# Optimization experiments

Hardware: AMD Instinct MI355X
Metric: run time of the kernel (lower is better)

Reference implementation:

```python
import jax, jax.numpy as jnp
import numpy as np

B, S, D, H = 2, 2048, 2048, 16
DH = D // H  # 128
EPS = 1e-6


def _rms_norm(x, w):
    # RMSNorm over last dim with learnable scale
    var = jnp.mean(jnp.square(x), axis=-1, keepdims=True)
    return x * jax.lax.rsqrt(var + EPS) * w


def _apply_rope(x, angles):
    # x: [B, S, H, DH]; angles: [S, DH//2]; interleaved pair rotation
    xs = x.reshape(*x.shape[:-1], DH // 2, 2)
    x0, x1 = xs[..., 0], xs[..., 1]
    cos = jnp.cos(angles)[None, :, None, :]  # [1,S,1,DH/2]
    sin = jnp.sin(angles)[None, :, None, :]
    r0 = x0 * cos - x1 * sin
    r1 = x0 * sin + x1 * cos
    return jnp.stack([r0, r1], axis=-1).reshape(x.shape)


def setup_inputs() -> dict:
    key = jax.random.key(0)
    ks = jax.random.split(key, 4)
    x = jax.random.normal(ks[0], (B, S, D), dtype=jnp.float32)
    # standard RoPE angle table: pos * inv_freq
    inv_freq = 1.0 / (10000.0 ** (jnp.arange(0, DH, 2, dtype=jnp.float32) / DH))
    pos = jnp.arange(S, dtype=jnp.float32)
    rp_freqs = pos[:, None] * inv_freq[None, :]  # [S, DH/2]
    Win = jax.random.normal(ks[1], (3 * D, D), dtype=jnp.float32) * (D ** -0.5)
    b_in = jnp.zeros((3 * D,), dtype=jnp.float32)
    Wout = jax.random.normal(ks[2], (D, D), dtype=jnp.float32) * (D ** -0.5)
    b_out = jnp.zeros((D,), dtype=jnp.float32)
    qk_w = jnp.ones((DH,), dtype=jnp.float32)
    out_w = jnp.ones((D,), dtype=jnp.float32)
    return {"x": x, "rp_freqs": rp_freqs, "Win": Win, "b_in": b_in,
            "Wout": Wout, "b_out": b_out, "qk_w": qk_w, "out_w": out_w}


def reference(x, rp_freqs, Win, b_in, Wout, b_out, qk_w, out_w):
    b, s, d = x.shape
    qkv = jnp.einsum('bsd,ed->bse', x, Win) + b_in  # [B,S,3D]
    qkv = qkv.reshape(b, s, 3, H, DH)
    q, k, v = qkv[:, :, 0], qkv[:, :, 1], qkv[:, :, 2]  # each [B,S,H,DH]
    q = _apply_rope(q, rp_freqs)
    k = _apply_rope(k, rp_freqs)
    q = _rms_norm(q, qk_w)
    k = _rms_norm(k, qk_w)
    # causal SDPA, scale = 1/sqrt(DH) (default)
    a = jax.nn.dot_product_attention(q, k, v, is_causal=True)  # [B,S,H,DH]
    a = a.reshape(b, s, d)
    a = _rms_norm(a, out_w)
    return jnp.einsum('bsd,ed->bse', a, Wout) + b_out
```

## Files before the change

kernel.cpp:

```cpp
#include <hip/hip_runtime.h>
#include <cstdint>
#include <cstddef>

#define Bq  2
#define Sq  2048
#define Dq  2048
#define Hq  16
#define DHq 128
#define E3q 6144

typedef __attribute__((ext_vector_type(8))) short s16x8;
typedef __attribute__((ext_vector_type(4))) float f32x4;

__device__ __forceinline__ unsigned short f2bf(float f){
  union { float f; unsigned u; } v; v.f = f;
  unsigned r = v.u + 0x7FFFu + ((v.u >> 16) & 1u);
  return (unsigned short)(r >> 16);
}
__device__ __forceinline__ float bf2f(unsigned short b){
  union { unsigned u; float f; } v; v.u = ((unsigned)b) << 16;
  return v.f;
}
__device__ __forceinline__ unsigned cvtpk_bf16(float lo, float hi){
  unsigned r;
  asm("v_cvt_pk_bf16_f32 %0, %1, %2" : "=v"(r) : "v"(lo), "v"(hi));
  return r;
}

__device__ __forceinline__ void gload_lds16(const void* g, void* l){
  __builtin_amdgcn_global_load_lds(
      (const __attribute__((address_space(1))) void*)g,
      (__attribute__((address_space(3))) void*)l, 16, 0, 0);
}

__global__ __launch_bounds__(256) void k_convert(const float* __restrict__ in,
                                                 unsigned short* __restrict__ out, int n4){
  int stride = gridDim.x * blockDim.x;
  for (int i = blockIdx.x*blockDim.x + threadIdx.x; i < n4; i += stride){
    float4 v = reinterpret_cast<const float4*>(in)[i];
    ushort4 o;
    o.x = f2bf(v.x); o.y = f2bf(v.y); o.z = f2bf(v.z); o.w = f2bf(v.w);
    reinterpret_cast<ushort4*>(out)[i] = o;
  }
}

__global__ __launch_bounds__(512, 1) void k_gemm1_8ph(const unsigned short* __restrict__ A,
                                                      const unsigned short* __restrict__ Bt,
                                                      const float* __restrict__ bias,
                                                      unsigned short* __restrict__ C){
  const int K = 2048, N = 6144;
  const int bid = blockIdx.x;
  const int xcd = bid & 7, u = bid >> 3;
  const int m0 = (xcd*4 + (u & 3)) * 128;
  const int n0 = (u >> 2) * 384;

  const int tid = threadIdx.x;
  const int lane = tid & 63, w = tid >> 6, g = lane >> 4, c = lane & 15;
  const int wm = w >> 2, wn = w & 3;

  __shared__ __align__(16) unsigned short L[65536];

  const int srow = tid >> 2, spc = tid & 3;
  const int ssw = (spc ^ ((srow >> 1) & 3)) << 3;
  const unsigned short* aSrc  = A  + (size_t)(m0 + srow      )*K + ssw;
  const unsigned short* bSrc0 = Bt + (size_t)(n0 + srow      )*K + ssw;
  const unsigned short* bSrc1 = Bt + (size_t)(n0 + srow + 128)*K + ssw;
  const unsigned short* bSrc2 = Bt + (size_t)(n0 + srow + 256)*K + ssw;

  auto stA = [&](int t, int h){
    gload_lds16(aSrc + t*64 + h*32, &L[((t&1)*2 + h)*4096 + tid*8]);
  };
  auto stB = [&](int t, int h, int uu){
    const unsigned short* s = (uu==0) ? bSrc0 : (uu==1) ? bSrc1 : bSrc2;
    gload_lds16(s + t*64 + h*32, &L[16384 + ((t&1)*2 + h)*12288 + uu*4096 + tid*8]);
  };

  int aoff[4], boff[6];
#pragma unroll
  for (int mf=0; mf<4; ++mf){
    int row = wm*64 + mf*16 + c;
    aoff[mf] = row*32 + ((g ^ ((row>>1)&3)) << 3);
  }
#pragma unroll
  for (int nf=0; nf<6; ++nf){
    int row = wn*96 + nf*16 + c;
    boff[nf] = row*32 + ((g ^ ((row>>1)&3)) << 3);
  }

  f32x4 acc[4][6];
#pragma unroll
  for (int i=0;i<4;i++)
#pragma unroll
    for (int j=0;j<6;j++)
#pragma unroll
      for (int r=0;r<4;r++) acc[i][j][r] = 0.f;

  auto RDA = [&](int b, int h, s16x8* af){
    const int ab = (b*2 + h)*4096;
#pragma unroll
    for (int mf=0; mf<4; ++mf) af[mf] = *(const s16x8*)&L[ab + aoff[mf]];
  };
  auto RDB = [&](int b, int h, int nh, s16x8* bf){
    const int bb = 16384 + (b*2 + h)*12288;
#pragma unroll
    for (int j=0; j<3; ++j) bf[j] = *(const s16x8*)&L[bb + boff[nh*3 + j]];
  };
  auto MM = [&](s16x8* af, s16x8* bf, int nh){
    __builtin_amdgcn_s_setprio(1);
#pragma unroll
    for (int mf=0; mf<4; ++mf)
#pragma unroll
      for (int j=0; j<3; ++j)
        acc[mf][nh*3+j] = __builtin_amdgcn_mfma_f32_16x16x32_bf16(af[mf], bf[j], acc[mf][nh*3+j], 0,0,0);
    __builtin_amdgcn_s_setprio(0);
  };
  auto BAR = [&](){
    __builtin_amdgcn_sched_barrier(0);
    __builtin_amdgcn_s_barrier();
    __builtin_amdgcn_sched_barrier(0);
  };

  stA(0,0); stB(0,0,0); stB(0,0,1); stB(0,0,2);
  stA(0,1); stB(0,1,0); stB(0,1,1); stB(0,1,2);
  stA(1,0); stB(1,0,0); stB(1,0,1); stB(1,0,2);
  asm volatile("s_waitcnt vmcnt(4)" ::: "memory");
  __builtin_amdgcn_s_barrier();

  for (int i=0; i<16; ++i){
    const int T0 = 2*i, T1 = 2*i + 1;
    const bool st = (i < 15);
    s16x8 af[4], bf[3];
    RDA(0,0,af); RDB(0,0,0,bf);
    stA(T1,1); stB(T1,1,0);
    BAR(); MM(af,bf,0); BAR();
    RDB(0,0,1,bf);
    stB(T1,1,1); stB(T1,1,2);
    BAR(); MM(af,bf,1); BAR();
    RDA(0,1,af); RDB(0,1,0,bf);
    if (st){ stA(T0+2,0); stB(T0+2,0,0); }
    BAR(); MM(af,bf,0); BAR();
    RDB(0,1,1,bf);
    if (st){ stB(T0+2,0,1); stB(T0+2,0,2); }
    __builtin_amdgcn_sched_barrier(0);
    if (st) asm volatile("s_waitcnt vmcnt(4)" ::: "memory");
    else    asm volatile("s_waitcnt vmcnt(0)" ::: "memory");
    BAR(); MM(af,bf,1); BAR();
    RDA(1,0,af); RDB(1,0,0,bf);
    if (st){ stA(T0+2,1); stB(T0+2,1,0); }
    BAR(); MM(af,bf,0); BAR();
    RDB(1,0,1,bf);
    if (st){ stB(T0+2,1,1); stB(T0+2,1,2); }
    BAR(); MM(af,bf,1); BAR();
    RDA(1,1,af); RDB(1,1,0,bf);
    if (st){ stA(T1+2,0); stB(T1+2,0,0); }
    BAR(); MM(af,bf,0); BAR();
    RDB(1,1,1,bf);
    if (st){ stB(T1+2,0,1); stB(T1+2,0,2); }
    __builtin_amdgcn_sched_barrier(0);
    if (st) asm volatile("s_waitcnt vmcnt(4)" ::: "memory");
    else    asm volatile("s_waitcnt vmcnt(0)" ::: "memory");
    BAR(); MM(af,bf,1); BAR();
  }

#pragma unroll
  for (int nf=0; nf<6; ++nf){
    const int col = n0 + wn*96 + nf*16 + c;
    const float bv = bias[col];
#pragma unroll
    for (int mf=0; mf<4; ++mf){
      const int row = m0 + wm*64 + mf*16 + g*4;
#pragma unroll
      for (int r=0; r<4; ++r)
        C[(size_t)(row+r)*N + col] = f2bf(acc[mf][nf][r] + bv);
    }
  }
}

template<int F32OUT>
__global__ __launch_bounds__(256, 2) void k_gemm_bt(const unsigned short* __restrict__ A,
                                                    const unsigned short* __restrict__ Bt,
                                                    const float* __restrict__ bias,
                                                    void* __restrict__ C,
                                                    int M, int N, int K){
  const int bid = blockIdx.x;
  const int xcd = bid & 7, u = bid >> 3;
  const int by = xcd*4 + (u & 3);
  const int bx = u >> 2;
  const int m0 = by * 128, n0 = bx * 256;

  const int tid = threadIdx.x;
  const int w = tid >> 6, lane = tid & 63, g = lane >> 4, c = lane & 15;

  __shared__ __align__(16) unsigned short L[3 * 12288];

  const int NT = K >> 5;

  const int r0 = tid >> 2, pc = tid & 3;
  const unsigned short* Ab0 = &A [(size_t)(m0 + r0      )*K + (size_t)((pc ^ (((r0      )>>1)&3))*8)];
  const unsigned short* Ab1 = &A [(size_t)(m0 + r0 +  64)*K + (size_t)((pc ^ (((r0 + 64)>>1)&3))*8)];
  const unsigned short* Bb0 = &Bt[(size_t)(n0 + r0      )*K + (size_t)((pc ^ (((r0      )>>1)&3))*8)];
  const unsigned short* Bb1 = &Bt[(size_t)(n0 + r0 +  64)*K + (size_t)((pc ^ (((r0 + 64)>>1)&3))*8)];
  const unsigned short* Bb2 = &Bt[(size_t)(n0 + r0 + 128)*K + (size_t)((pc ^ (((r0 +128)>>1)&3))*8)];
  const unsigned short* Bb3 = &Bt[(size_t)(n0 + r0 + 192)*K + (size_t)((pc ^ (((r0 +192)>>1)&3))*8)];

  auto stage = [&](int tile, int slot){
    const int kt = tile << 5;
    unsigned short* Ls = &L[slot * 12288];
    gload_lds16(Ab0 + kt, &Ls[tid*8]);
    gload_lds16(Ab1 + kt, &Ls[(tid+256)*8]);
    gload_lds16(Bb0 + kt, &Ls[4096 + tid*8]);
    gload_lds16(Bb1 + kt, &Ls[4096 + (tid+256)*8]);
    gload_lds16(Bb2 + kt, &Ls[4096 + (tid+512)*8]);
    gload_lds16(Bb3 + kt, &Ls[4096 + (tid+768)*8]);
  };

  f32x4 acc[8][4];
#pragma unroll
  for (int i=0;i<8;i++)
#pragma unroll
    for (int j=0;j<4;j++)
#pragma unroll
      for (int r=0;r<4;r++) acc[i][j][r] = 0.f;

  int aoff[8], boff[4];
#pragma unroll
  for (int mi=0;mi<8;mi++){
    int row = mi*16 + c;
    aoff[mi] = row*32 + ((g ^ ((row>>1)&3)) << 3);
  }
#pragma unroll
  for (int ni=0;ni<4;ni++){
    int row = w*64 + ni*16 + c;
    boff[ni] = 4096 + row*32 + ((g ^ ((row>>1)&3)) << 3);
  }

  stage(0,0); stage(1,1);

  int slot = 0;
  for (int t = 0; t < NT; ++t){
    if (t < NT-1) asm volatile("s_waitcnt vmcnt(6)" ::: "memory");
    else          asm volatile("s_waitcnt vmcnt(0)" ::: "memory");
    __builtin_amdgcn_s_barrier();
    __builtin_amdgcn_sched_barrier(0);
    if (t+2 < NT) stage(t+2, slot == 0 ? 2 : slot-1);

    const unsigned short* Ls = &L[slot * 12288];
    s16x8 bfr[4];
#pragma unroll
    for (int ni=0;ni<4;ni++) bfr[ni] = *(const s16x8*)&Ls[boff[ni]];
    __builtin_amdgcn_s_setprio(1);
#pragma unroll
    for (int mi=0;mi<8;mi++){
      s16x8 af = *(const s16x8*)&Ls[aoff[mi]];
#pragma unroll
      for (int ni=0;ni<4;ni++)
        acc[mi][ni] = __builtin_amdgcn_mfma_f32_16x16x32_bf16(af, bfr[ni], acc[mi][ni], 0,0,0);
    }
    __builtin_amdgcn_s_setprio(0);
    slot = (slot == 2) ? 0 : slot+1;
  }

#pragma unroll
  for (int ni=0;ni<4;ni++){
    const int col = n0 + w*64 + ni*16 + c;
    const float bv = bias[col];
#pragma unroll
    for (int mi=0;mi<8;mi++){
      const int row = m0 + mi*16 + g*4;
#pragma unroll
      for (int r=0;r<4;r++){
        float v = acc[mi][ni][r] + bv;
        if (F32OUT) ((float*)C)[(size_t)(row+r)*N + col] = v;
        else ((unsigned short*)C)[(size_t)(row+r)*N + col] = f2bf(v);
      }
    }
  }
}

__global__ __launch_bounds__(256) void k_rope_qk(const unsigned short* __restrict__ QKV,
                                                 const float* __restrict__ rp,
                                                 const float* __restrict__ qk_w,
                                                 unsigned short* __restrict__ Qp,
                                                 unsigned short* __restrict__ Kp){
  const int p = threadIdx.x;
  const int s = blockIdx.x*4 + threadIdx.y;
  const int h = blockIdx.y;
  const int b = blockIdx.z;
  const size_t n = (size_t)b*Sq + s;
  const int bh = b*Hq + h;

  float ang = rp[s*64 + p];
  float sn, cs; sincosf(ang, &sn, &cs);
  float w0 = qk_w[2*p], w1 = qk_w[2*p+1];
  const float QSCALE = 0.08838834764831845f * 1.4426950408889634f;

  {
    unsigned q01 = *(const unsigned*)&QKV[n*E3q + h*DHq + 2*p];
    float x0 = bf2f((unsigned short)(q01 & 0xFFFFu));
    float x1 = bf2f((unsigned short)(q01 >> 16));
    float r0 = x0*cs - x1*sn, r1 = x0*sn + x1*cs;
    float ss = r0*r0 + r1*r1;
#pragma unroll
    for (int m=1;m<64;m<<=1) ss += __shfl_xor(ss, m);
    float sc = rsqrtf(ss/128.f + 1e-6f) * QSCALE;
    unsigned short o0 = f2bf(r0*sc*w0), o1 = f2bf(r1*sc*w1);
    *(unsigned*)&Qp[((size_t)bh*Sq + s)*DHq + 2*p] = (unsigned)o0 | ((unsigned)o1<<16);
  }
  {
    unsigned k01 = *(const unsigned*)&QKV[n*E3q + Dq + h*DHq + 2*p];
    float x0 = bf2f((unsigned short)(k01 & 0xFFFFu));
    float x1 = bf2f((unsigned short)(k01 >> 16));
    float r0 = x0*cs - x1*sn, r1 = x0*sn + x1*cs;
    float ss = r0*r0 + r1*r1;
#pragma unroll
    for (int m=1;m<64;m<<=1) ss += __shfl_xor(ss, m);
    float sc = rsqrtf(ss/128.f + 1e-6f);
    unsigned short o0 = f2bf(r0*sc*w0), o1 = f2bf(r1*sc*w1);
    *(unsigned*)&Kp[((size_t)bh*Sq + s)*DHq + 2*p] = (unsigned)o0 | ((unsigned)o1<<16);
  }
}

__global__ __launch_bounds__(256) void k_transpose_v(const unsigned short* __restrict__ QKV,
                                                     unsigned short* __restrict__ Vt){
  const int sblk = blockIdx.x;
  const int bh = blockIdx.y;
  const int b = bh >> 4, h = bh & 15;
  const int tid = threadIdx.x;
  __shared__ unsigned short T[128][136];

  const size_t base = ((size_t)(b*Sq) + sblk*128) * E3q + 2*(size_t)Dq + h*DHq;
#pragma unroll
  for (int i=0;i<8;i++){
    int pk = tid + i*256;
    int row = pk >> 4, cc = (pk & 15) * 8;
    s16x8 v = *(const s16x8*)&QKV[base + (size_t)row*E3q + cc];
    *(s16x8*)&T[row][cc] = v;
  }
  __syncthreads();
  const int dh = tid >> 1, sh = (tid & 1) * 64;
  unsigned short buf[64];
#pragma unroll
  for (int s=0;s<64;s++) buf[s] = T[sh + s][dh];
  size_t obase = ((size_t)bh*DHq + dh)*Sq + sblk*128 + sh;
#pragma unroll
  for (int i=0;i<8;i++)
    *(s16x8*)&Vt[obase + i*8] = *(const s16x8*)&buf[i*8];
}

__global__ __launch_bounds__(256, 2) void k_attn(const unsigned short* __restrict__ Qp,
                                                 const unsigned short* __restrict__ Kp,
                                                 const unsigned short* __restrict__ Vt,
                                                 unsigned short* __restrict__ Ar){
  const int L = blockIdx.x;
  int bh, qtile;
  if (L < 256){ bh = L >> 3; qtile = 8 + (L & 7); }
  else { int Ml = L - 256; bh = Ml >> 3; qtile = 7 - (Ml & 7); }
  const int b = bh >> 4, h = bh & 15;
  const int tid = threadIdx.x;
  const int w = tid >> 6, lane = tid & 63, g = lane >> 4, c = lane & 15;
  const int r0w = qtile*128 + w*32;

  const unsigned short* Qh = Qp + (size_t)bh * Sq * DHq;
  const unsigned short* Kh = Kp + (size_t)bh * Sq * DHq;
  const unsigned short* Vh = Vt + (size_t)bh * DHq * Sq;

  __shared__ __align__(16) unsigned short Ks[2][64*128];
  __shared__ __align__(16) unsigned short Vs[2][128*64];
  __shared__ __align__(16) unsigned short Pl[4][32*64];
  unsigned short* Pw = &Pl[w][0];

  s16x8 qf[2][4];
#pragma unroll
  for (int mi=0;mi<2;mi++)
#pragma unroll
    for (int kc=0;kc<4;kc++)
      qf[mi][kc] = *(const s16x8*)&Qh[(size_t)(r0w + mi*16 + c)*DHq + kc*32 + g*8];

  f32x4 acc[2][8];
#pragma unroll
  for (int mi=0;mi<2;mi++)
#pragma unroll
    for (int dt=0;dt<8;dt++)
#pragma unroll
      for (int r=0;r<4;r++) acc[mi][dt][r] = 0.f;
  float m_r[2] = { -INFINITY, -INFINITY };
  float l_p[2] = { 0.f, 0.f };

  const int nsteps = 2*qtile + 2;

  auto stage = [&](int j0s, int bufi){
#pragma unroll
    for (int i=0;i<4;i++){
      int pk = tid + i*256;
      int row = pk>>4, pcc = pk&15;
      gload_lds16(&Kh[(size_t)(j0s+row)*DHq + ((pcc^(row&7))<<3)], &Ks[bufi][pk*8]);
    }
#pragma unroll
    for (int i=0;i<4;i++){
      int pk = tid + i*256;
      int row = pk>>3, pcc = pk&7;
      gload_lds16(&Vh[(size_t)row*Sq + j0s + ((pcc^(row&7))<<3)], &Vs[bufi][pk*8]);
    }
  };

  stage(0, 0);
  __syncthreads();

  for (int t=0; t<nsteps; ++t){
    const int j0 = t*64;
    if (t+1 < nsteps) stage((t+1)*64, (t+1)&1);

    if (j0 <= r0w + 31){
      const unsigned short* Kc = &Ks[t&1][0];
      const unsigned short* Vc = &Vs[t&1][0];

      f32x4 sv[2][4];
#pragma unroll
      for (int mi=0;mi<2;mi++)
#pragma unroll
        for (int js=0;js<4;js++)
#pragma unroll
          for (int r=0;r<4;r++) sv[mi][js][r] = 0.f;

      __builtin_amdgcn_s_setprio(1);
#pragma unroll
      for (int js=0;js<4;js++){
        s16x8 kf[4];
#pragma unroll
        for (int kc=0;kc<4;kc++)
          kf[kc] = *(const s16x8*)&Kc[(js*16 + c)*128 + (((kc*4+g)^(c&7))<<3)];
#pragma unroll
        for (int mi=0;mi<2;mi++)
#pragma unroll
          for (int kc=0;kc<4;kc++)
            sv[mi][js] = __builtin_amdgcn_mfma_f32_16x16x32_bf16(kf[kc], qf[mi][kc], sv[mi][js], 0,0,0);
      }
      __builtin_amdgcn_s_setprio(0);

      if (j0 + 63 > r0w){
#pragma unroll
        for (int mi=0;mi<2;mi++){
          const int q = r0w + mi*16 + c;
#pragma unroll
          for (int js=0;js<4;js++)
#pragma unroll
            for (int r=0;r<4;r++)
              if (j0 + js*16 + g*4 + r > q) sv[mi][js][r] = -INFINITY;
        }
      }

      float pmx[2];
#pragma unroll
      for (int mi=0;mi<2;mi++){
        float mx = fmaxf(fmaxf(sv[mi][0][0],sv[mi][0][1]), fmaxf(sv[mi][0][2],sv[mi][0][3]));
#pragma unroll
        for (int js=1;js<4;js++){
          float a = fmaxf(fmaxf(sv[mi][js][0],sv[mi][js][1]), fmaxf(sv[mi][js][2],sv[mi][js][3]));
          mx = fmaxf(mx, a);
        }
        mx = fmaxf(mx, __shfl_xor(mx, 16));
        mx = fmaxf(mx, __shfl_xor(mx, 32));
        pmx[mi] = mx;
      }
      int need = (pmx[0] > m_r[0] + 8.f) | (pmx[1] > m_r[1] + 8.f);
      if (__any(need)){
#pragma unroll
        for (int mi=0;mi<2;mi++){
          float mnew = fmaxf(m_r[mi], pmx[mi]);
          float corr = exp2f(m_r[mi] - mnew);
          l_p[mi] *= corr;
          m_r[mi] = mnew;
#pragma unroll
          for (int dt=0;dt<8;dt++)
#pragma unroll
            for (int r=0;r<4;r++) acc[mi][dt][r] *= corr;
        }
      }
#pragma unroll
      for (int mi=0;mi<2;mi++){
        const float mm = m_r[mi];
        const int rowoff = (mi*16 + c)*64;
#pragma unroll
        for (int js=0;js<4;js++){
          float e0 = exp2f(sv[mi][js][0] - mm);
          float e1 = exp2f(sv[mi][js][1] - mm);
          float e2 = exp2f(sv[mi][js][2] - mm);
          float e3 = exp2f(sv[mi][js][3] - mm);
          l_p[mi] += (e0+e1)+(e2+e3);
          uint2 pk2;
          pk2.x = cvtpk_bf16(e0, e1);
          pk2.y = cvtpk_bf16(e2, e3);
          const int kc8 = js*2 + (g>>1);
          *(uint2*)&Pw[rowoff + ((kc8 ^ (c&7))<<3) + (g&1)*4] = pk2;
        }
      }

      s16x8 pfr[2][2];
#pragma unroll
      for (int mi=0;mi<2;mi++)
#pragma unroll
        for (int kc=0;kc<2;kc++)
          pfr[mi][kc] = *(const s16x8*)&Pw[(mi*16 + c)*64 + (((kc*4+g)^(c&7))<<3)];
      __builtin_amdgcn_s_setprio(1);
#pragma unroll
      for (int dt=0; dt<8; dt++){
#pragma unroll
        for (int kc=0;kc<2;kc++){
          s16x8 vfr = *(const s16x8*)&Vc[(dt*16 + c)*64 + (((kc*4+g)^(c&7))<<3)];
#pragma unroll
          for (int mi=0;mi<2;mi++)
            acc[mi][dt] = __builtin_amdgcn_mfma_f32_16x16x32_bf16(vfr, pfr[mi][kc], acc[mi][dt], 0,0,0);
        }
      }
      __builtin_amdgcn_s_setprio(0);
    }
    __syncthreads();
  }

#pragma unroll
  for (int mi=0;mi<2;mi++){
    float l = l_p[mi];
    l += __shfl_xor(l, 16);
    l += __shfl_xor(l, 32);
    const float inv = 1.f / l;
    const int row = r0w + mi*16 + c;
    unsigned short* dst = &Ar[((size_t)(b*Sq + row))*Dq + h*DHq];
#pragma unroll
    for (int dt=0; dt<8; dt++){
      uint2 o2;
      o2.x = cvtpk_bf16(acc[mi][dt][0]*inv, acc[mi][dt][1]*inv);
      o2.y = cvtpk_bf16(acc[mi][dt][2]*inv, acc[mi][dt][3]*inv);
      *(uint2*)&dst[dt*16 + g*4] = o2;
    }
  }
}

__global__ __launch_bounds__(256) void k_rmsnorm(unsigned short* __restrict__ A,
                                                 const float* __restrict__ w){
  const int row = blockIdx.x;
  const int tid = threadIdx.x;
  s16x8 v = *(const s16x8*)&A[(size_t)row*Dq + tid*8];
  float f[8]; float ss = 0.f;
#pragma unroll
  for (int i=0;i<8;i++){ f[i] = bf2f((unsigned short)v[i]); ss += f[i]*f[i]; }
#pragma unroll
  for (int m=1;m<64;m<<=1) ss += __shfl_xor(ss, m);
  __shared__ float red[4];
  if ((tid&63)==0) red[tid>>6] = ss;
  __syncthreads();
  ss = red[0]+red[1]+red[2]+red[3];
  float sc = rsqrtf(ss/2048.f + 1e-6f);
  unsigned short o[8];
#pragma unroll
  for (int i=0;i<8;i++) o[i] = f2bf(f[i]*sc*w[tid*8+i]);
  *(s16x8*)&A[(size_t)row*Dq + tid*8] = *(const s16x8*)o;
}

extern "C" void kernel_launch(void* const* d_in, const int* in_sizes, int n_in,
                              void* d_out, int out_size, void* d_ws, size_t ws_size,
                              hipStream_t stream){
  const float* x     = (const float*)d_in[0];
  const float* rp    = (const float*)d_in[1];
  const float* Win   = (const float*)d_in[2];
  const float* b_in  = (const float*)d_in[3];
  const float* Wout  = (const float*)d_in[4];
  const float* b_out = (const float*)d_in[5];
  const float* qk_w  = (const float*)d_in[6];
  const float* out_w = (const float*)d_in[7];
  float* outp = (float*)d_out;

  if (ws_size < (160ull<<20)) return;

  char* ws = (char*)d_ws;
  unsigned short* Xb    = (unsigned short*)(ws);
  unsigned short* Wb    = (unsigned short*)(ws + (16ull<<20));
  unsigned short* Woutb = (unsigned short*)(ws + (40ull<<20));
  unsigned short* QKVb  = (unsigned short*)(ws + (48ull<<20));
  unsigned short* Qp    = (unsigned short*)(ws + (96ull<<20));
  unsigned short* Kp    = (unsigned short*)(ws + (112ull<<20));
  unsigned short* Vt    = (unsigned short*)(ws + (128ull<<20));
  unsigned short* Ar    = (unsigned short*)(ws + (144ull<<20));

  k_convert<<<2048, 256, 0, stream>>>(x,    Xb,    (Bq*Sq*Dq)/4);
  k_convert<<<2048, 256, 0, stream>>>(Win,  Wb,    (E3q*Dq)/4);
  k_convert<<<1024, 256, 0, stream>>>(Wout, Woutb, (Dq*Dq)/4);
  k_gemm1_8ph<<<512, 512, 0, stream>>>(Xb, Wb, b_in, QKVb);
  k_rope_qk<<<dim3(Sq/4, Hq, Bq), dim3(64,4), 0, stream>>>(QKVb, rp, qk_w, Qp, Kp);
  k_transpose_v<<<dim3(Sq/128, Bq*Hq), 256, 0, stream>>>(QKVb, Vt);
  k_attn<<<512, 256, 0, stream>>>(Qp, Kp, Vt, Ar);
  k_rmsnorm<<<Bq*Sq, 256, 0, stream>>>(Ar, out_w);
  k_gemm_bt<1><<<256, 256, 0, stream>>>(Ar, Woutb, b_out, outp, Bq*Sq, Dq, Dq);
}
```

Before: 288.1 us.

## Pipeline output GEMM with 8-phase 512-thread schedule and fuse input conversions

The output projection GEMM now uses a 512-thread, 8-wave kernel. Each iteration is split into eight phases that interleave LDS reads, global-to-LDS prefetches of the next K tiles, and MFMA groups between barriers, mirroring the QKV GEMM design. Separately, the three fp32-to-bf16 conversion launches are merged into a single grid-stride kernel to remove launch overhead and tail effects. The new GEMM gives each wave a smaller per-wave tile and adds many barriers, and it assumes fixed problem dimensions.

```diff
diff --git a/kernel.cpp b/kernel.cpp
--- a/kernel.cpp
+++ b/kernel.cpp
@@ -33,14 +33,26 @@
       (__attribute__((address_space(3))) void*)l, 16, 0, 0);
 }
 
-__global__ __launch_bounds__(256) void k_convert(const float* __restrict__ in,
-                                                 unsigned short* __restrict__ out, int n4){
+__global__ __launch_bounds__(256) void k_convert3(const float* __restrict__ x,
+                                                  const float* __restrict__ win,
+                                                  const float* __restrict__ wout,
+                                                  unsigned short* __restrict__ xb,
+                                                  unsigned short* __restrict__ wb,
+                                                  unsigned short* __restrict__ woutb){
+  const int NX = (Bq*Sq*Dq)/4;
+  const int NW = (E3q*Dq)/4;
+  const int NO = (Dq*Dq)/4;
+  const int total = NX + NW + NO;
   int stride = gridDim.x * blockDim.x;
-  for (int i = blockIdx.x*blockDim.x + threadIdx.x; i < n4; i += stride){
-    float4 v = reinterpret_cast<const float4*>(in)[i];
+  for (int i = blockIdx.x*blockDim.x + threadIdx.x; i < total; i += stride){
+    const float* src; unsigned short* dst; int j;
+    if (i < NX){ src = x; dst = xb; j = i; }
+    else if (i < NX+NW){ src = win; dst = wb; j = i - NX; }
+    else { src = wout; dst = woutb; j = i - NX - NW; }
+    float4 v = reinterpret_cast<const float4*>(src)[j];
     ushort4 o;
     o.x = f2bf(v.x); o.y = f2bf(v.y); o.z = f2bf(v.z); o.w = f2bf(v.w);
-    reinterpret_cast<ushort4*>(out)[i] = o;
+    reinterpret_cast<ushort4*>(dst)[j] = o;
   }
 }
 
@@ -176,103 +188,133 @@
   }
 }
 
-template<int F32OUT>
-__global__ __launch_bounds__(256, 2) void k_gemm_bt(const unsigned short* __restrict__ A,
-                                                    const unsigned short* __restrict__ Bt,
-                                                    const float* __restrict__ bias,
-                                                    void* __restrict__ C,
-                                                    int M, int N, int K){
+__global__ __launch_bounds__(512, 1) void k_gemm2_8ph(const unsigned short* __restrict__ A,
+                                                      const unsigned short* __restrict__ Bt,
+                                                      const float* __restrict__ bias,
+                                                      float* __restrict__ C){
+  const int K = 2048, N = 2048, NI = 16;
   const int bid = blockIdx.x;
   const int xcd = bid & 7, u = bid >> 3;
-  const int by = xcd*4 + (u & 3);
-  const int bx = u >> 2;
-  const int m0 = by * 128, n0 = bx * 256;
+  const int m0 = (xcd*4 + (u & 3)) * 128;
+  const int n0 = (u >> 2) * 256;
 
   const int tid = threadIdx.x;
-  const int w = tid >> 6, lane = tid & 63, g = lane >> 4, c = lane & 15;
-
-  __shared__ __align__(16) unsigned short L[3 * 12288];
-
-  const int NT = K >> 5;
-
-  const int r0 = tid >> 2, pc = tid & 3;
-  const unsigned short* Ab0 = &A [(size_t)(m0 + r0      )*K + (size_t)((pc ^ (((r0      )>>1)&3))*8)];
-  const unsigned short* Ab1 = &A [(size_t)(m0 + r0 +  64)*K + (size_t)((pc ^ (((r0 + 64)>>1)&3))*8)];
-  const unsigned short* Bb0 = &Bt[(size_t)(n0 + r0      )*K + (size_t)((pc ^ (((r0      )>>1)&3))*8)];
-  const unsigned short* Bb1 = &Bt[(size_t)(n0 + r0 +  64)*K + (size_t)((pc ^ (((r0 + 64)>>1)&3))*8)];
-  const unsigned short* Bb2 = &Bt[(size_t)(n0 + r0 + 128)*K + (size_t)((pc ^ (((r0 +128)>>1)&3))*8)];
-  const unsigned short* Bb3 = &Bt[(size_t)(n0 + r0 + 192)*K + (size_t)((pc ^ (((r0 +192)>>1)&3))*8)];
-
-  auto stage = [&](int tile, int slot){
-    const int kt = tile << 5;
-    unsigned short* Ls = &L[slot * 12288];
-    gload_lds16(Ab0 + kt, &Ls[tid*8]);
-    gload_lds16(Ab1 + kt, &Ls[(tid+256)*8]);
-    gload_lds16(Bb0 + kt, &Ls[4096 + tid*8]);
-    gload_lds16(Bb1 + kt, &Ls[4096 + (tid+256)*8]);
-    gload_lds16(Bb2 + kt, &Ls[4096 + (tid+512)*8]);
-    gload_lds16(Bb3 + kt, &Ls[4096 + (tid+768)*8]);
-  };
-
-  f32x4 acc[8][4];
-#pragma unroll
-  for (int i=0;i<8;i++)
+  const int lane = tid & 63, w = tid >> 6, g = lane >> 4, c = lane & 15;
+  const int wm = w >> 2, wn = w & 3;
+
+  __shared__ __align__(16) unsigned short L[49152];
+
+  const int srow = tid >> 2, spc = tid & 3;
+  const int ssw = (spc ^ ((srow >> 1) & 3)) << 3;
+  const unsigned short* aSrc  = A  + (size_t)(m0 + srow      )*K + ssw;
+  const unsigned short* bSrc0 = Bt + (size_t)(n0 + srow      )*K + ssw;
+  const unsigned short* bSrc1 = Bt + (size_t)(n0 + srow + 128)*K + ssw;
+
+  auto stA = [&](int t, int h){
+    gload_lds16(aSrc + t*64 + h*32, &L[((t&1)*2 + h)*4096 + tid*8]);
+  };
+  auto stB = [&](int t, int h, int uu){
+    const unsigned short* s = (uu==0) ? bSrc0 : bSrc1;
+    gload_lds16(s + t*64 + h*32, &L[16384 + ((t&1)*2 + h)*8192 + uu*4096 + tid*8]);
+  };
+
+  int aoff[4], boff[4];
+#pragma unroll
+  for (int mf=0; mf<4; ++mf){
+    int row = wm*64 + mf*16 + c;
+    aoff[mf] = row*32 + ((g ^ ((row>>1)&3)) << 3);
+  }
+#pragma unroll
+  for (int nf=0; nf<4; ++nf){
+    int row = wn*64 + nf*16 + c;
+    boff[nf] = row*32 + ((g ^ ((row>>1)&3)) << 3);
+  }
+
+  f32x4 acc[4][4];
+#pragma unroll
+  for (int i=0;i<4;i++)
 #pragma unroll
     for (int j=0;j<4;j++)
 #pragma unroll
       for (int r=0;r<4;r++) acc[i][j][r] = 0.f;
 
-  int aoff[8], boff[4];
-#pragma unroll
-  for (int mi=0;mi<8;mi++){
-    int row = mi*16 + c;
-    aoff[mi] = row*32 + ((g ^ ((row>>1)&3)) << 3);
-  }
-#pragma unroll
-  for (int ni=0;ni<4;ni++){
-    int row = w*64 + ni*16 + c;
-    boff[ni] = 4096 + row*32 + ((g ^ ((row>>1)&3)) << 3);
-  }
-
-  stage(0,0); stage(1,1);
-
-  int slot = 0;
-  for (int t = 0; t < NT; ++t){
-    if (t < NT-1) asm volatile("s_waitcnt vmcnt(6)" ::: "memory");
-    else          asm volatile("s_waitcnt vmcnt(0)" ::: "memory");
+  auto RDA = [&](int b, int h, s16x8* af){
+    const int ab = (b*2 + h)*4096;
+#pragma unroll
+    for (int mf=0; mf<4; ++mf) af[mf] = *(const s16x8*)&L[ab + aoff[mf]];
+  };
+  auto RDB = [&](int b, int h, int nh, s16x8* bf){
+    const int bb = 16384 + (b*2 + h)*8192;
+#pragma unroll
+    for (int j=0; j<2; ++j) bf[j] = *(const s16x8*)&L[bb + boff[nh*2 + j]];
+  };
+  auto MM = [&](s16x8* af, s16x8* bf, int nh){
+    __builtin_amdgcn_s_setprio(1);
+#pragma unroll
+    for (int mf=0; mf<4; ++mf)
+#pragma unroll
+      for (int j=0; j<2; ++j)
+        acc[mf][nh*2+j] = __builtin_amdgcn_mfma_f32_16x16x32_bf16(af[mf], bf[j], acc[mf][nh*2+j], 0,0,0);
+    __builtin_amdgcn_s_setprio(0);
+  };
+  auto BAR = [&](){
+    __builtin_amdgcn_sched_barrier(0);
     __builtin_amdgcn_s_barrier();
     __builtin_amdgcn_sched_barrier(0);
-    if (t+2 < NT) stage(t+2, slot == 0 ? 2 : slot-1);
-
-    const unsigned short* Ls = &L[slot * 12288];
-    s16x8 bfr[4];
-#pragma unroll
-    for (int ni=0;ni<4;ni++) bfr[ni] = *(const s16x8*)&Ls[boff[ni]];
-    __builtin_amdgcn_s_setprio(1);
-#pragma unroll
-    for (int mi=0;mi<8;mi++){
-      s16x8 af = *(const s16x8*)&Ls[aoff[mi]];
-#pragma unroll
-      for (int ni=0;ni<4;ni++)
-        acc[mi][ni] = __builtin_amdgcn_mfma_f32_16x16x32_bf16(af, bfr[ni], acc[mi][ni], 0,0,0);
-    }
-    __builtin_amdgcn_s_setprio(0);
-    slot = (slot == 2) ? 0 : slot+1;
-  }
-
-#pragma unroll
-  for (int ni=0;ni<4;ni++){
-    const int col = n0 + w*64 + ni*16 + c;
+  };
+
+  stA(0,0); stB(0,0,0); stB(0,0,1);
+  stA(0,1); stB(0,1,0); stB(0,1,1);
+  stA(1,0); stB(1,0,0); stB(1,0,1);
+  asm volatile("s_waitcnt vmcnt(3)" ::: "memory");
+  __builtin_amdgcn_s_barrier();
+
+  for (int i=0; i<NI; ++i){
+    const int T0 = 2*i, T1 = 2*i + 1;
+    const bool st = (i < NI-1);
+    s16x8 af[4], bf[2];
+    RDA(0,0,af); RDB(0,0,0,bf);
+    stA(T1,1); stB(T1,1,0);
+    BAR(); MM(af,bf,0); BAR();
+    RDB(0,0,1,bf);
+    stB(T1,1,1);
+    BAR(); MM(af,bf,1); BAR();
+    RDA(0,1,af); RDB(0,1,0,bf);
+    if (st){ stA(T0+2,0); stB(T0+2,0,0); }
+    BAR(); MM(af,bf,0); BAR();
+    RDB(0,1,1,bf);
+    if (st){ stB(T0+2,0,1); }
+    __builtin_amdgcn_sched_barrier(0);
+    if (st) asm volatile("s_waitcnt vmcnt(3)" ::: "memory");
+    else    asm volatile("s_waitcnt vmcnt(0)" ::: "memory");
+    BAR(); MM(af,bf,1); BAR();
+    RDA(1,0,af); RDB(1,0,0,bf);
+    if (st){ stA(T0+2,1); stB(T0+2,1,0); }
+    BAR(); MM(af,bf,0); BAR();
+    RDB(1,0,1,bf);
+    if (st){ stB(T0+2,1,1); }
+    BAR(); MM(af,bf,1); BAR();
+    RDA(1,1,af); RDB(1,1,0,bf);
+    if (st){ stA(T1+2,0); stB(T1+2,0,0); }
+    BAR(); MM(af,bf,0); BAR();
+    RDB(1,1,1,bf);
+    if (st){ stB(T1+2,0,1); }
+    __builtin_amdgcn_sched_barrier(0);
+    if (st) asm volatile("s_waitcnt vmcnt(3)" ::: "memory");
+    else    asm volatile("s_waitcnt vmcnt(0)" ::: "memory");
+    BAR(); MM(af,bf,1); BAR();
+  }
+
+#pragma unroll
+  for (int nf=0; nf<4; ++nf){
+    const int col = n0 + wn*64 + nf*16 + c;
     const float bv = bias[col];
 #pragma unroll
-    for (int mi=0;mi<8;mi++){
-      const int row = m0 + mi*16 + g*4;
-#pragma unroll
-      for (int r=0;r<4;r++){
-        float v = acc[mi][ni][r] + bv;
-        if (F32OUT) ((float*)C)[(size_t)(row+r)*N + col] = v;
-        else ((unsigned short*)C)[(size_t)(row+r)*N + col] = f2bf(v);
-      }
+    for (int mf=0; mf<4; ++mf){
+      const int row = m0 + wm*64 + mf*16 + g*4;
+#pragma unroll
+      for (int r=0; r<4; ++r)
+        C[(size_t)(row+r)*N + col] = acc[mf][nf][r] + bv;
     }
   }
 }
@@ -581,13 +623,11 @@
   unsigned short* Vt    = (unsigned short*)(ws + (128ull<<20));
   unsigned short* Ar    = (unsigned short*)(ws + (144ull<<20));
 
-  k_convert<<<2048, 256, 0, stream>>>(x,    Xb,    (Bq*Sq*Dq)/4);
-  k_convert<<<2048, 256, 0, stream>>>(Win,  Wb,    (E3q*Dq)/4);
-  k_convert<<<1024, 256, 0, stream>>>(Wout, Woutb, (Dq*Dq)/4);
+  k_convert3<<<2048, 256, 0, stream>>>(x, Win, Wout, Xb, Wb, Woutb);
   k_gemm1_8ph<<<512, 512, 0, stream>>>(Xb, Wb, b_in, QKVb);
   k_rope_qk<<<dim3(Sq/4, Hq, Bq), dim3(64,4), 0, stream>>>(QKVb, rp, qk_w, Qp, Kp);
   k_transpose_v<<<dim3(Sq/128, Bq*Hq), 256, 0, stream>>>(QKVb, Vt);
   k_attn<<<512, 256, 0, stream>>>(Qp, Kp, Vt, Ar);
   k_rmsnorm<<<Bq*Sq, 256, 0, stream>>>(Ar, out_w);
-  k_gemm_bt<1><<<256, 256, 0, stream>>>(Ar, Woutb, b_out, outp, Bq*Sq, Dq, Dq);
-}
+  k_gemm2_8ph<<<256, 512, 0, stream>>>(Ar, Woutb, b_out, outp);
+}
```

Measured after the change: 278.0 us. 1.04x faster.
